# Kernel tuning notes

Hardware: AMD Instinct MI355X
Metric: run time of the kernel (lower is better)

## Reference

```python
import jax, jax.numpy as jnp
import numpy as np

NUM_ITERS = 3
NUM_HEADS = 4
EPS = 1e-8
LN_EPS = 1e-5


def _layernorm(x, w, b):
    mu = jnp.mean(x, axis=-1, keepdims=True)
    var = jnp.mean(jnp.square(x - mu), axis=-1, keepdims=True)
    return (x - mu) * jax.lax.rsqrt(var + LN_EPS) * w + b


def setup_inputs() -> dict:
    key = jax.random.key(0)
    ks = jax.random.split(key, 12)
    B, K, D, Q, Hm = 64, 4096, 256, 8, 512
    s = 0.02
    return {
        "inputs": jax.random.normal(ks[0], (B, K, D), jnp.float32),
        "slots_init": jax.random.normal(ks[1], (B, Q, D), jnp.float32),
        "Wq": jax.random.normal(ks[2], (D, D), jnp.float32) * s,
        "Wk": jax.random.normal(ks[3], (D, D), jnp.float32) * s,
        "Wv": jax.random.normal(ks[4], (D, D), jnp.float32) * s,
        "ln_in_w": jnp.ones((D,), jnp.float32),
        "ln_in_b": jnp.zeros((D,), jnp.float32),
        "ln_slots_w": jnp.ones((D,), jnp.float32),
        "ln_slots_b": jnp.zeros((D,), jnp.float32),
        "ln_mlp_w": jnp.ones((D,), jnp.float32),
        "ln_mlp_b": jnp.zeros((D,), jnp.float32),
        "gru_Wih": jax.random.normal(ks[5], (3 * D, D), jnp.float32) * s,
        "gru_Whh": jax.random.normal(ks[6], (3 * D, D), jnp.float32) * s,
        "gru_bih": jnp.zeros((3 * D,), jnp.float32),
        "gru_bhh": jnp.zeros((3 * D,), jnp.float32),
        "mlp_W1": jax.random.normal(ks[7], (D, Hm), jnp.float32) * s,
        "mlp_b1": jnp.zeros((Hm,), jnp.float32),
        "mlp_W2": jax.random.normal(ks[8], (Hm, D), jnp.float32) * s,
        "mlp_b2": jnp.zeros((D,), jnp.float32),
    }


def reference(inputs, slots_init, Wq, Wk, Wv, ln_in_w, ln_in_b, ln_slots_w,
              ln_slots_b, ln_mlp_w, ln_mlp_b, gru_Wih, gru_Whh, gru_bih,
              gru_bhh, mlp_W1, mlp_b1, mlp_W2, mlp_b2):
    B, K, D = inputs.shape
    Q = slots_init.shape[1]
    H = NUM_HEADS
    dh = D // H
    scale = dh ** -0.5

    x = _layernorm(inputs, ln_in_w, ln_in_b)
    k = (x @ Wk).reshape(B, K, H, dh).transpose(0, 2, 1, 3) * scale  # [B,H,K,dh]
    v = (x @ Wv).reshape(B, K, H, dh).transpose(0, 2, 1, 3)          # [B,H,K,dh]

    slots = slots_init
    attn = None
    for _ in range(NUM_ITERS):
        slots_prev = slots
        s_n = _layernorm(slots, ln_slots_w, ln_slots_b)
        q = (s_n @ Wq).reshape(B, Q, H, dh).transpose(0, 2, 1, 3)    # [B,H,Q,dh]
        logits = jnp.einsum('bhkd,bhqd->bhkq', k, q)                 # [B,H,K,Q]
        # softmax jointly over (heads, slots) per kv position
        attn = jax.nn.softmax(
            logits.transpose(0, 2, 1, 3).reshape(B, K, H * Q), axis=-1
        ).reshape(B, K, H, Q).transpose(0, 2, 1, 3)                  # [B,H,K,Q]
        attn = attn + EPS
        attn = attn / jnp.sum(attn, axis=2, keepdims=True)           # renorm over K
        updates = jnp.einsum('bhkq,bhkd->bqhd', attn, v).reshape(B, Q, D)

        # GRU cell (PyTorch gate order: r, z, n)
        u = updates.reshape(-1, D)
        h = slots_prev.reshape(-1, D)
        gi = u @ gru_Wih.T + gru_bih
        gh = h @ gru_Whh.T + gru_bhh
        i_r, i_z, i_n = jnp.split(gi, 3, axis=-1)
        h_r, h_z, h_n = jnp.split(gh, 3, axis=-1)
        r = jax.nn.sigmoid(i_r + h_r)
        z = jax.nn.sigmoid(i_z + h_z)
        n = jnp.tanh(i_n + r * h_n)
        slots = ((1.0 - z) * n + z * h).reshape(B, Q, D)

        m = _layernorm(slots, ln_mlp_w, ln_mlp_b)
        slots = slots + jax.nn.relu(m @ mlp_W1 + mlp_b1) @ mlp_W2 + mlp_b2

    return slots, attn.mean(axis=1).transpose(0, 2, 1)  # [B,Q,D], [B,Q,K]
```

## Files before the change

kernel.cpp:

```cpp
#include <hip/hip_runtime.h>

#define B   64
#define KK  4096
#define D   256
#define Q   8
#define H   4
#define DH  64
#define HQ  32
#define HM  512
#define NCH 8
#define CHK 512
#define EPS 1e-8f
#define LNE 1e-5f
#define SCALE 0.125f

typedef short bf16x8 __attribute__((ext_vector_type(8)));
typedef float f32x4 __attribute__((ext_vector_type(4)));

__device__ __forceinline__ float bf2f(unsigned short u) {
    unsigned int x = ((unsigned int)u) << 16;
    float f; __builtin_memcpy(&f, &x, 4); return f;
}
__device__ __forceinline__ unsigned short f2bf(float f) {
    unsigned int x; __builtin_memcpy(&x, &f, 4);
    unsigned int lsb = (x >> 16) & 1u;
    x += 0x7fffu + lsb;
    return (unsigned short)(x >> 16);
}

__device__ __forceinline__ void gload16(const void* g, void* l) {
    __builtin_amdgcn_global_load_lds(
        (const __attribute__((address_space(1))) unsigned int*)g,
        (__attribute__((address_space(3))) unsigned int*)l, 16, 0, 0);
}

__device__ __forceinline__ void stage64x512B(const char* src, size_t row0,
                                             size_t stride, char* lds, int w, int l)
{
#pragma unroll
    for (int i = 0; i < 8; ++i) {
        const int seg = w * 8 + i;
        const int r = seg * 2 + (l >> 5);
        const int off = ((l & 31) * 16) ^ ((r & 7) << 4);
        gload16(src + (row0 + r) * stride + off, lds + seg * 1024);
    }
}

__global__ void k_init(const float* __restrict__ s0, float* __restrict__ slots,
                       unsigned short* __restrict__ slots_bf)
{
    const int i = blockIdx.x * 256 + threadIdx.x;
    const float v = s0[i];
    slots[i] = v; slots_bf[i] = f2bf(v);
}

__global__ __launch_bounds__(256) void k0_wkv(
    const float* __restrict__ Wk, const float* __restrict__ Wv,
    unsigned short* __restrict__ WkvT)
{
    const int c = blockIdx.x, d = threadIdx.x;
    const float v = (c < 256) ? Wk[(size_t)d * 256 + c] * SCALE
                              : Wv[(size_t)d * 256 + (c - 256)];
    WkvT[(size_t)c * 256 + d] = f2bf(v);
}

__global__ void k0_cvt(const float* __restrict__ src, unsigned short* __restrict__ dst)
{
    const int i = blockIdx.x * 256 + threadIdx.x;
    dst[i] = f2bf(src[i]);
}

__global__ void k0_t1(const float* __restrict__ W1, unsigned short* __restrict__ W1T)
{
    const int n = blockIdx.x, d = threadIdx.x;
    W1T[(size_t)n * 256 + d] = f2bf(W1[(size_t)d * 512 + n]);
}

__global__ void k0_t2(const float* __restrict__ W2, unsigned short* __restrict__ W2T)
{
    const int n = blockIdx.x, j = threadIdx.x;
    W2T[(size_t)n * 512 + j]       = f2bf(W2[(size_t)j * 256 + n]);
    W2T[(size_t)n * 512 + 256 + j] = f2bf(W2[(size_t)(256 + j) * 256 + n]);
}

__global__ __launch_bounds__(256) void k1_mfma(
    const float* __restrict__ inp, const unsigned short* __restrict__ WkvT,
    const float* __restrict__ lnw, const float* __restrict__ lnb,
    unsigned short* __restrict__ kbuf, unsigned short* __restrict__ vbufT)
{
    __shared__ char smem[65536];
    char* abase = smem;
    char* bb0 = smem + 32768;
    char* bb1 = smem;
    const int t = threadIdx.x, w = t >> 6, l = t & 63;
    const size_t row0 = (size_t)blockIdx.x * 64;

    float4 xv[16];
#pragma unroll
    for (int i = 0; i < 16; ++i)
        xv[i] = ((const float4*)(inp + (row0 + w * 16 + i) * D))[l];
    const float4 w4 = ((const float4*)lnw)[l];
    const float4 b4 = ((const float4*)lnb)[l];
#pragma unroll
    for (int i = 0; i < 16; ++i) {
        const int r = w * 16 + i;
        float4 x = xv[i];
        float s  = x.x + x.y + x.z + x.w;
        float ss = x.x*x.x + x.y*x.y + x.z*x.z + x.w*x.w;
#pragma unroll
        for (int off = 32; off; off >>= 1) { s += __shfl_xor(s, off); ss += __shfl_xor(ss, off); }
        const float mu = s * (1.f / 256.f);
        const float rs = rsqrtf(ss * (1.f / 256.f) - mu * mu + LNE);
        ushort4 pk;
        pk.x = f2bf((x.x - mu) * rs * w4.x + b4.x);
        pk.y = f2bf((x.y - mu) * rs * w4.y + b4.y);
        pk.z = f2bf((x.z - mu) * rs * w4.z + b4.z);
        pk.w = f2bf((x.w - mu) * rs * w4.w + b4.w);
        *(ushort4*)(abase + r * 512 + ((l * 8) ^ ((r & 7) << 4))) = pk;
    }
    __syncthreads();

    const int arow = w * 16 + (l & 15);
    const char* ap = abase + arow * 512;
    const int asw = (l & 7) << 4;
    bf16x8 af[8];
#pragma unroll
    for (int kk = 0; kk < 8; ++kk)
        af[kk] = *(const bf16x8*)(ap + ((kk * 64 + (l >> 4) * 16) ^ asw));

    stage64x512B((const char*)WkvT, 0, 512, bb0, w, l);
    __syncthreads();

    const f32x4 fz = {0.f, 0.f, 0.f, 0.f};
    for (int n2 = 0; n2 < 8; ++n2) {
        if (n2 < 7)
            stage64x512B((const char*)WkvT, (size_t)(n2 + 1) * 64, 512,
                         ((n2 + 1) & 1) ? bb1 : bb0, w, l);
        const char* bbase = (n2 & 1) ? bb1 : bb0;
        f32x4 acc[4] = {fz, fz, fz, fz};
#pragma unroll
        for (int kk = 0; kk < 8; ++kk) {
            const int koff = kk * 64 + (l >> 4) * 16;
#pragma unroll
            for (int nf = 0; nf < 4; ++nf) {
                const int brow = nf * 16 + (l & 15);
                const bf16x8 bf_ = *(const bf16x8*)(bbase + brow * 512 + (koff ^ ((brow & 7) << 4)));
                acc[nf] = __builtin_amdgcn_mfma_f32_16x16x32_bf16(af[kk], bf_, acc[nf], 0, 0, 0);
            }
        }
        const int c0 = n2 * 64;
        const size_t grow0 = row0 + w * 16 + (l >> 4) * 4;
#pragma unroll
        for (int nf = 0; nf < 4; ++nf) {
            const int c = c0 + nf * 16 + (l & 15);
            if (c < 256) {
#pragma unroll
                for (int reg = 0; reg < 4; ++reg)
                    kbuf[(grow0 + reg) * 256 + c] = f2bf(acc[nf][reg]);
            } else {
                const int cc = c - 256;
                const size_t bb = grow0 >> 12;
                const int kl = (int)(grow0 & 4095);
                ushort4 pk;
                pk.x = f2bf(acc[nf][0]); pk.y = f2bf(acc[nf][1]);
                pk.z = f2bf(acc[nf][2]); pk.w = f2bf(acc[nf][3]);
                *(ushort4*)(vbufT + ((bb * 256 + cc) * KK + kl)) = pk;
            }
        }
        __syncthreads();
    }
}

__global__ __launch_bounds__(256) void k2_qproj(
    const float* __restrict__ slots, const float* __restrict__ Wq,
    const float* __restrict__ lnw, const float* __restrict__ lnb, float* __restrict__ qbuf)
{
    const int row = blockIdx.x, t = threadIdx.x;
    __shared__ float sn[256];
    __shared__ float red[8];
    const float x = slots[(size_t)row * D + t];
    float mu, rs;
    {
        float s = x, ss = x * x;
#pragma unroll
        for (int off = 32; off; off >>= 1) { s += __shfl_xor(s, off); ss += __shfl_xor(ss, off); }
        if ((t & 63) == 0) { red[t >> 6] = s; red[4 + (t >> 6)] = ss; }
        __syncthreads();
        const float S  = red[0] + red[1] + red[2] + red[3];
        const float SS = red[4] + red[5] + red[6] + red[7];
        mu = S * (1.f / 256.f);
        rs = rsqrtf(SS * (1.f / 256.f) - mu * mu + LNE);
    }
    sn[t] = (x - mu) * rs * lnw[t] + lnb[t];
    __syncthreads();
    float acc = 0.f;
    for (int d = 0; d < 256; ++d) acc = fmaf(sn[d], Wq[(size_t)d * 256 + t], acc);
    qbuf[(size_t)row * D + t] = acc;
}

__global__ __launch_bounds__(256) void k_attn(
    const unsigned short* __restrict__ kbuf, const unsigned short* __restrict__ vbufT,
    const float* __restrict__ qbuf, float* __restrict__ updp,
    float* __restrict__ denp, float* __restrict__ pbuf, int write_p)
{
    __shared__ unsigned short ksm[64 * 256];
    __shared__ unsigned short vsm[256 * 64];
    __shared__ unsigned short psm[32 * 64];
    __shared__ float dred[4][32];
    const int t = threadIdx.x, w = t >> 6, l = t & 63;
    const int b = blockIdx.x >> 3, chunk = blockIdx.x & 7;
    const int k0g = chunk * CHK;
    const int n = l & 15, lg = l >> 4;

    auto stage_ks = [&](int tile) {
        const size_t rowg = (size_t)b * KK + k0g + tile * 64;
#pragma unroll
        for (int i = 0; i < 8; ++i) {
            const int seg = w * 8 + i;
            const int r = seg * 2 + (l >> 5);
            const int off = ((l & 31) * 16) ^ ((r & 7) << 4);
            gload16((const char*)kbuf + (rowg + r) * 512 + off, (char*)ksm + seg * 1024);
        }
    };
    auto stage_vs = [&](int tile) {
        const int kk0 = k0g + tile * 64;
#pragma unroll
        for (int i = 0; i < 8; ++i) {
            const int seg = w * 8 + i;
            const int d = seg * 8 + (l >> 3);
            const int off = ((l & 7) * 16) ^ ((d & 7) << 4);
            gload16((const char*)vbufT + (((size_t)b * 256 + d) * KK + kk0) * 2 + off,
                    (char*)vsm + seg * 1024);
        }
    };
    stage_ks(0); stage_vs(0);

    bf16x8 qf[2][2];
#pragma unroll
    for (int p = 0; p < 2; ++p) {
        const int h = p * 2 + (n >> 3);
        const float* qb = qbuf + ((size_t)b * Q + (n & 7)) * D;
#pragma unroll
        for (int j = 0; j < 2; ++j) {
            const int dbase = (h * 2 + j) * 32 + lg * 8;
            short tmp[8];
#pragma unroll
            for (int e = 0; e < 8; ++e) tmp[e] = (short)f2bf(qb[dbase + e]);
            __builtin_memcpy(&qf[p][j], tmp, 16);
        }
    }
    const bf16x8 ZV = {0,0,0,0,0,0,0,0};
    const f32x4 fz = {0.f,0.f,0.f,0.f};
    f32x4 pv[2][4];
#pragma unroll
    for (int mt = 0; mt < 2; ++mt)
#pragma unroll
        for (int nf = 0; nf < 4; ++nf) pv[mt][nf] = fz;
    float den0 = 0.f, den1 = 0.f;

    for (int tile = 0; tile < 8; ++tile) {
        __syncthreads();
        const int arow = w * 16 + n;
        const char* ap = (const char*)ksm + arow * 512;
        const int asw = (arow & 7) << 4;
        f32x4 lac[2] = {fz, fz};
#pragma unroll
        for (int kk = 0; kk < 8; ++kk) {
            const bf16x8 a = *(const bf16x8*)(ap + ((kk * 64 + lg * 16) ^ asw));
            const int p = kk >> 2;
            const bool on = (((kk & 3) >> 1) == (n >> 3));
            const bf16x8 bq = on ? qf[p][kk & 1] : ZV;
            if (p == 0) lac[0] = __builtin_amdgcn_mfma_f32_16x16x32_bf16(a, bq, lac[0], 0, 0, 0);
            else        lac[1] = __builtin_amdgcn_mfma_f32_16x16x32_bf16(a, bq, lac[1], 0, 0, 0);
        }
#pragma unroll
        for (int reg = 0; reg < 4; ++reg) {
            float m = fmaxf(lac[0][reg], lac[1][reg]);
#pragma unroll
            for (int off = 8; off; off >>= 1) m = fmaxf(m, __shfl_xor(m, off));
            const float e0 = __expf(lac[0][reg] - m);
            const float e1 = __expf(lac[1][reg] - m);
            float se = e0 + e1;
#pragma unroll
            for (int off = 8; off; off >>= 1) se += __shfl_xor(se, off);
            const float inv = 1.f / se;
            lac[0][reg] = e0 * inv; lac[1][reg] = e1 * inv;
            den0 += lac[0][reg];    den1 += lac[1][reg];
        }
        const int kb = w * 16 + lg * 4;
        {
            ushort4 p0, p1;
            p0.x = f2bf(lac[0][0]); p0.y = f2bf(lac[0][1]); p0.z = f2bf(lac[0][2]); p0.w = f2bf(lac[0][3]);
            p1.x = f2bf(lac[1][0]); p1.y = f2bf(lac[1][1]); p1.z = f2bf(lac[1][2]); p1.w = f2bf(lac[1][3]);
            *(ushort4*)((char*)psm + n * 128 + ((kb * 2) ^ ((n & 7) << 4))) = p0;
            *(ushort4*)((char*)psm + (16 + n) * 128 + ((kb * 2) ^ ((n & 7) << 4))) = p1;
        }
        if (write_p) {
            float* pp = pbuf + ((size_t)b * KK + k0g + tile * 64 + kb) * HQ;
#pragma unroll
            for (int reg = 0; reg < 4; ++reg) {
                pp[(size_t)reg * HQ + n] = lac[0][reg];
                pp[(size_t)reg * HQ + 16 + n] = lac[1][reg];
            }
        }
        __syncthreads();
        if (tile < 7) stage_ks(tile + 1);
#pragma unroll
        for (int kk = 0; kk < 2; ++kk) {
            const int koff = kk * 64 + lg * 16;
            const bf16x8 a0 = *(const bf16x8*)((char*)psm + n * 128 + (koff ^ ((n & 7) << 4)));
            const bf16x8 a1 = *(const bf16x8*)((char*)psm + (16 + n) * 128 + (koff ^ ((n & 7) << 4)));
#pragma unroll
            for (int nf = 0; nf < 4; ++nf) {
                const int d = w * 64 + nf * 16 + n;
                const bf16x8 bv = *(const bf16x8*)((char*)vsm + d * 128 + (koff ^ ((d & 7) << 4)));
                pv[0][nf] = __builtin_amdgcn_mfma_f32_16x16x32_bf16(a0, bv, pv[0][nf], 0, 0, 0);
                pv[1][nf] = __builtin_amdgcn_mfma_f32_16x16x32_bf16(a1, bv, pv[1][nf], 0, 0, 0);
            }
        }
        __syncthreads();
        if (tile < 7) stage_vs(tile + 1);
    }

    den0 += __shfl_xor(den0, 16); den0 += __shfl_xor(den0, 32);
    den1 += __shfl_xor(den1, 16); den1 += __shfl_xor(den1, 32);
    if (l < 16) { dred[w][l] = den0; dred[w][16 + l] = den1; }
    __syncthreads();
    if (t < 32)
        denp[((size_t)b * NCH + chunk) * HQ + t] =
            dred[0][t] + dred[1][t] + dred[2][t] + dred[3][t];

    if ((lg >> 1) == (w & 1)) {
        const int mt = w >> 1;
#pragma unroll
        for (int nf = 0; nf < 4; ++nf) {
#pragma unroll
            for (int reg = 0; reg < 4; ++reg) {
                const int q = (lg & 1) * 4 + reg;
                updp[(((size_t)b * NCH + chunk) * Q + q) * D + w * 64 + nf * 16 + n] = pv[mt][nf][reg];
            }
        }
    }
}

__global__ __launch_bounds__(256) void k_reduce(
    const float* __restrict__ updp, const float* __restrict__ denp,
    unsigned short* __restrict__ updbf)
{
    const int row = blockIdx.x, t = threadIdx.x;
    const int b = row >> 3, q = row & 7, h = t >> 6;
    float ds = 0.f, us = 0.f;
#pragma unroll
    for (int c = 0; c < NCH; ++c) {
        ds += denp[((size_t)b * NCH + c) * HQ + h * Q + q];
        us += updp[(((size_t)b * NCH + c) * Q + q) * D + t];
    }
    updbf[(size_t)row * D + t] = f2bf(us / (ds + (float)KK * EPS));
}

__global__ void k_den(const float* __restrict__ denp, float* __restrict__ invden)
{
    const int b = blockIdx.x, t = threadIdx.x;
    float s = 0.f;
#pragma unroll
    for (int c = 0; c < NCH; ++c) s += denp[((size_t)b * NCH + c) * HQ + t];
    invden[b * HQ + t] = 1.f / (s + (float)KK * EPS);
}

__global__ __launch_bounds__(256) void k_gru(
    const unsigned short* __restrict__ updbf, const unsigned short* __restrict__ slotsbf,
    const unsigned short* __restrict__ Wihbf, const unsigned short* __restrict__ Whhbf,
    float* __restrict__ gg)
{
    __shared__ unsigned short As[64 * 256];
    __shared__ unsigned short Bs[64 * 256];
    const int t = threadIdx.x, w = t >> 6, l = t & 63;
    const int rb = blockIdx.x / 24, nb = blockIdx.x % 24;
    const unsigned short* Asrc = (nb < 12) ? updbf : slotsbf;
    stage64x512B((const char*)Asrc, (size_t)rb * 64, 512, (char*)As, w, l);
    if (nb < 12) stage64x512B((const char*)Wihbf, (size_t)nb * 64, 512, (char*)Bs, w, l);
    else         stage64x512B((const char*)Whhbf, (size_t)(nb - 12) * 64, 512, (char*)Bs, w, l);
    __syncthreads();
    const int arow = w * 16 + (l & 15);
    const int asw = (l & 7) << 4;
    bf16x8 af[8];
#pragma unroll
    for (int kk = 0; kk < 8; ++kk)
        af[kk] = *(const bf16x8*)((char*)As + arow * 512 + ((kk * 64 + (l >> 4) * 16) ^ asw));
    const f32x4 fz = {0.f,0.f,0.f,0.f};
    f32x4 acc[4] = {fz, fz, fz, fz};
#pragma unroll
    for (int kk = 0; kk < 8; ++kk) {
        const int koff = kk * 64 + (l >> 4) * 16;
#pragma unroll
        for (int nf = 0; nf < 4; ++nf) {
            const int brow = nf * 16 + (l & 15);
            const bf16x8 bf_ = *(const bf16x8*)((char*)Bs + brow * 512 + (koff ^ ((brow & 7) << 4)));
            acc[nf] = __builtin_amdgcn_mfma_f32_16x16x32_bf16(af[kk], bf_, acc[nf], 0, 0, 0);
        }
    }
    const int colbase = (nb < 12) ? nb * 64 : 768 + (nb - 12) * 64;
#pragma unroll
    for (int nf = 0; nf < 4; ++nf) {
        const int col = colbase + nf * 16 + (l & 15);
#pragma unroll
        for (int reg = 0; reg < 4; ++reg) {
            const size_t row = (size_t)rb * 64 + w * 16 + (l >> 4) * 4 + reg;
            gg[row * 1536 + col] = acc[nf][reg];
        }
    }
}

__global__ __launch_bounds__(256) void k_gates(
    const float* __restrict__ gg, const float* __restrict__ slots,
    const float* __restrict__ bih, const float* __restrict__ bhh,
    const float* __restrict__ lnw, const float* __restrict__ lnb,
    float* __restrict__ snew, unsigned short* __restrict__ mbf)
{
    const int row = blockIdx.x, t = threadIdx.x;
    __shared__ float red[8];
    const float* g = gg + (size_t)row * 1536;
    const float i_r = g[t]        + bih[t];
    const float i_z = g[256 + t]  + bih[256 + t];
    const float i_n = g[512 + t]  + bih[512 + t];
    const float h_r = g[768 + t]  + bhh[t];
    const float h_z = g[1024 + t] + bhh[256 + t];
    const float h_n = g[1280 + t] + bhh[512 + t];
    const float r = 1.f / (1.f + __expf(-(i_r + h_r)));
    const float z = 1.f / (1.f + __expf(-(i_z + h_z)));
    const float nn = tanhf(i_n + r * h_n);
    const float h0 = slots[(size_t)row * D + t];
    const float sn = (1.f - z) * nn + z * h0;
    snew[(size_t)row * D + t] = sn;
    float mu, rs;
    {
        float s = sn, ss = sn * sn;
#pragma unroll
        for (int off = 32; off; off >>= 1) { s += __shfl_xor(s, off); ss += __shfl_xor(ss, off); }
        if ((t & 63) == 0) { red[t >> 6] = s; red[4 + (t >> 6)] = ss; }
        __syncthreads();
        const float S  = red[0] + red[1] + red[2] + red[3];
        const float SS = red[4] + red[5] + red[6] + red[7];
        mu = S * (1.f / 256.f);
        rs = rsqrtf(SS * (1.f / 256.f) - mu * mu + LNE);
    }
    mbf[(size_t)row * D + t] = f2bf((sn - mu) * rs * lnw[t] + lnb[t]);
}

__global__ __launch_bounds__(256) void k_mlp1(
    const unsigned short* __restrict__ mbf, const unsigned short* __restrict__ W1T,
    const float* __restrict__ b1, unsigned short* __restrict__ hidbf)
{
    __shared__ unsigned short As[64 * 256];
    __shared__ unsigned short Bs[64 * 256];
    const int t = threadIdx.x, w = t >> 6, l = t & 63;
    const int rb = blockIdx.x >> 3, nb = blockIdx.x & 7;
    stage64x512B((const char*)mbf, (size_t)rb * 64, 512, (char*)As, w, l);
    stage64x512B((const char*)W1T, (size_t)nb * 64, 512, (char*)Bs, w, l);
    __syncthreads();
    const int arow = w * 16 + (l & 15);
    const int asw = (l & 7) << 4;
    bf16x8 af[8];
#pragma unroll
    for (int kk = 0; kk < 8; ++kk)
        af[kk] = *(const bf16x8*)((char*)As + arow * 512 + ((kk * 64 + (l >> 4) * 16) ^ asw));
    const f32x4 fz = {0.f,0.f,0.f,0.f};
    f32x4 acc[4] = {fz, fz, fz, fz};
#pragma unroll
    for (int kk = 0; kk < 8; ++kk) {
        const int koff = kk * 64 + (l >> 4) * 16;
#pragma unroll
        for (int nf = 0; nf < 4; ++nf) {
            const int brow = nf * 16 + (l & 15);
            const bf16x8 bf_ = *(const bf16x8*)((char*)Bs + brow * 512 + (koff ^ ((brow & 7) << 4)));
            acc[nf] = __builtin_amdgcn_mfma_f32_16x16x32_bf16(af[kk], bf_, acc[nf], 0, 0, 0);
        }
    }
#pragma unroll
    for (int nf = 0; nf < 4; ++nf) {
        const int col = nb * 64 + nf * 16 + (l & 15);
        const float bb = b1[col];
#pragma unroll
        for (int reg = 0; reg < 4; ++reg) {
            const size_t row = (size_t)rb * 64 + w * 16 + (l >> 4) * 4 + reg;
            hidbf[row * HM + col] = f2bf(fmaxf(acc[nf][reg] + bb, 0.f));
        }
    }
}

__global__ __launch_bounds__(256) void k_mlp2(
    const unsigned short* __restrict__ hidbf, const unsigned short* __restrict__ W2T,
    const float* __restrict__ b2, const float* __restrict__ snew,
    float* __restrict__ slots, unsigned short* __restrict__ slotsbf)
{
    __shared__ unsigned short As[64 * 256];
    __shared__ unsigned short Bs[64 * 256];
    const int t = threadIdx.x, w = t >> 6, l = t & 63;
    const int rb = blockIdx.x >> 2, nb = blockIdx.x & 3;
    const f32x4 fz = {0.f,0.f,0.f,0.f};
    f32x4 acc[4] = {fz, fz, fz, fz};
    for (int c = 0; c < 2; ++c) {
        stage64x512B((const char*)hidbf + c * 512, (size_t)rb * 64, 1024, (char*)As, w, l);
        stage64x512B((const char*)W2T + c * 512, (size_t)nb * 64, 1024, (char*)Bs, w, l);
        __syncthreads();
        const int arow = w * 16 + (l & 15);
        const int asw = (l & 7) << 4;
        bf16x8 af[8];
#pragma unroll
        for (int kk = 0; kk < 8; ++kk)
            af[kk] = *(const bf16x8*)((char*)As + arow * 512 + ((kk * 64 + (l >> 4) * 16) ^ asw));
#pragma unroll
        for (int kk = 0; kk < 8; ++kk) {
            const int koff = kk * 64 + (l >> 4) * 16;
#pragma unroll
            for (int nf = 0; nf < 4; ++nf) {
                const int brow = nf * 16 + (l & 15);
                const bf16x8 bf_ = *(const bf16x8*)((char*)Bs + brow * 512 + (koff ^ ((brow & 7) << 4)));
                acc[nf] = __builtin_amdgcn_mfma_f32_16x16x32_bf16(af[kk], bf_, acc[nf], 0, 0, 0);
            }
        }
        __syncthreads();
    }
#pragma unroll
    for (int nf = 0; nf < 4; ++nf) {
        const int col = nb * 64 + nf * 16 + (l & 15);
        const float bb = b2[col];
#pragma unroll
        for (int reg = 0; reg < 4; ++reg) {
            const size_t row = (size_t)rb * 64 + w * 16 + (l >> 4) * 4 + reg;
            const float v = snew[row * D + col] + acc[nf][reg] + bb;
            slots[row * D + col] = v;
            slotsbf[row * D + col] = f2bf(v);
        }
    }
}

__global__ void k7_copy(const float* __restrict__ s, float* __restrict__ o)
{
    const int i = blockIdx.x * 256 + threadIdx.x;
    o[i] = s[i];
}

__global__ __launch_bounds__(256) void k7_attnout(
    const float* __restrict__ pbuf, const float* __restrict__ invden, float* __restrict__ out2)
{
    const int blk = blockIdx.x;
    const int b = blk >> 4;
    const int kk0 = (blk & 15) * 256;
    __shared__ float ps[256][33];
    __shared__ float inv[32];
    const int t = threadIdx.x;
    const float* pp = pbuf + ((size_t)b * KK + kk0) * HQ;
    for (int i = 0; i < 32; ++i) {
        const int idx = i * 256 + t;
        ps[idx >> 5][idx & 31] = pp[idx];
    }
    if (t < 32) inv[t] = invden[b * HQ + t];
// ... 22 lines not shown
    const float* ln_in_b = (const float*)d_in[6];
    const float* ln_s_w  = (const float*)d_in[7];
    const float* ln_s_b  = (const float*)d_in[8];
    const float* ln_m_w  = (const float*)d_in[9];
    const float* ln_m_b  = (const float*)d_in[10];
    const float* gWih    = (const float*)d_in[11];
    const float* gWhh    = (const float*)d_in[12];
    const float* gbih    = (const float*)d_in[13];
    const float* gbhh    = (const float*)d_in[14];
    const float* W1      = (const float*)d_in[15];
    const float* b1      = (const float*)d_in[16];
    const float* W2      = (const float*)d_in[17];
    const float* b2      = (const float*)d_in[18];

    char* p = (char*)d_ws;
    unsigned short* kbuf  = (unsigned short*)p; p += (size_t)B * KK * D * 2;
    unsigned short* vbufT = (unsigned short*)p; p += (size_t)B * KK * D * 2;
    float* pbuf   = (float*)p; p += (size_t)B * KK * HQ * 4;
    float* updp   = (float*)p; p += (size_t)B * NCH * Q * D * 4;
    float* denp   = (float*)p; p += (size_t)B * NCH * HQ * 4;
    float* invden = (float*)p; p += (size_t)B * HQ * 4;
    float* qbuf   = (float*)p; p += (size_t)B * Q * D * 4;
    float* slots  = (float*)p; p += (size_t)B * Q * D * 4;
    float* snew   = (float*)p; p += (size_t)B * Q * D * 4;
    unsigned short* slots_bf = (unsigned short*)p; p += (size_t)B * Q * D * 2;
    unsigned short* upd_bf   = (unsigned short*)p; p += (size_t)B * Q * D * 2;
    unsigned short* mbf      = (unsigned short*)p; p += (size_t)B * Q * D * 2;
    unsigned short* hidbf    = (unsigned short*)p; p += (size_t)B * Q * HM * 2;
    unsigned short* WkvT     = (unsigned short*)p; p += (size_t)512 * 256 * 2;
    unsigned short* Wihbf    = (unsigned short*)p; p += (size_t)768 * 256 * 2;
    unsigned short* Whhbf    = (unsigned short*)p; p += (size_t)768 * 256 * 2;
    unsigned short* W1T      = (unsigned short*)p; p += (size_t)HM * 256 * 2;
    unsigned short* W2T      = (unsigned short*)p; p += (size_t)256 * HM * 2;
    float* gg = updp;

    k_init<<<(B * Q * D) / 256, 256, 0, stream>>>(slots0, slots, slots_bf);
    k0_wkv<<<512, 256, 0, stream>>>(Wk, Wv, WkvT);
    k0_cvt<<<768, 256, 0, stream>>>(gWih, Wihbf);
    k0_cvt<<<768, 256, 0, stream>>>(gWhh, Whhbf);
    k0_t1<<<512, 256, 0, stream>>>(W1, W1T);
    k0_t2<<<256, 256, 0, stream>>>(W2, W2T);
    k1_mfma<<<(B * KK) / 64, 256, 0, stream>>>(inputs, WkvT, ln_in_w, ln_in_b, kbuf, vbufT);
    for (int it = 0; it < 3; ++it) {
        k2_qproj<<<B * Q, 256, 0, stream>>>(slots, Wq, ln_s_w, ln_s_b, qbuf);
        k_attn<<<B * NCH, 256, 0, stream>>>(kbuf, vbufT, qbuf, updp, denp, pbuf, (it == 2) ? 1 : 0);
        k_reduce<<<B * Q, 256, 0, stream>>>(updp, denp, upd_bf);
        k_gru<<<8 * 24, 256, 0, stream>>>(upd_bf, slots_bf, Wihbf, Whhbf, gg);
        k_gates<<<B * Q, 256, 0, stream>>>(gg, slots, gbih, gbhh, ln_m_w, ln_m_b, snew, mbf);
        k_mlp1<<<8 * 8, 256, 0, stream>>>(mbf, W1T, b1, hidbf);
        k_mlp2<<<8 * 4, 256, 0, stream>>>(hidbf, W2T, b2, snew, slots, slots_bf);
    }
    k_den<<<B, 32, 0, stream>>>(denp, invden);
    k7_copy<<<(B * Q * D) / 256, 256, 0, stream>>>(slots, (float*)d_out);
    k7_attnout<<<B * (KK / 256), 256, 0, stream>>>(pbuf, invden, (float*)d_out + (size_t)B * Q * D);
}
```

Measured before the change: 464.2 us.

## Fuse slot-update chain into one kernel and restructure attention loads

Folds the per-iteration reduce, GRU GEMMs, gates, MLP, and next-iteration Q projection into a single k_slot kernel of 32 blocks, replacing six launches per iteration. The attention kernel now uses 16 chunks of 256 keys and reads K and V fragments straight from global memory instead of staging them through LDS. The K/V projection kernel uses 32-column B tiles with a deeper prefetch and less shared memory. The aim is to cut launch overhead and intermediate global round-trips and raise attention parallelism, at the cost of a low-parallelism fused slot kernel and uncoalesced direct global loads in attention.

```diff
diff --git a/kernel.cpp b/kernel.cpp
--- a/kernel.cpp
+++ b/kernel.cpp
@@ -8,14 +8,16 @@
 #define DH  64
 #define HQ  32
 #define HM  512
-#define NCH 8
-#define CHK 512
+#define NCH 16
+#define CHK 256
 #define EPS 1e-8f
 #define LNE 1e-5f
 #define SCALE 0.125f
 
 typedef short bf16x8 __attribute__((ext_vector_type(8)));
 typedef float f32x4 __attribute__((ext_vector_type(4)));
+
+#define MFMA __builtin_amdgcn_mfma_f32_16x16x32_bf16
 
 __device__ __forceinline__ float bf2f(unsigned short u) {
     unsigned int x = ((unsigned int)u) << 16;
@@ -34,24 +36,10 @@
         (__attribute__((address_space(3))) unsigned int*)l, 16, 0, 0);
 }
 
-__device__ __forceinline__ void stage64x512B(const char* src, size_t row0,
-                                             size_t stride, char* lds, int w, int l)
-{
-#pragma unroll
-    for (int i = 0; i < 8; ++i) {
-        const int seg = w * 8 + i;
-        const int r = seg * 2 + (l >> 5);
-        const int off = ((l & 31) * 16) ^ ((r & 7) << 4);
-        gload16(src + (row0 + r) * stride + off, lds + seg * 1024);
-    }
-}
-
-__global__ void k_init(const float* __restrict__ s0, float* __restrict__ slots,
-                       unsigned short* __restrict__ slots_bf)
+__global__ void k_init(const float* __restrict__ s0, float* __restrict__ slots)
 {
     const int i = blockIdx.x * 256 + threadIdx.x;
-    const float v = s0[i];
-    slots[i] = v; slots_bf[i] = f2bf(v);
+    slots[i] = s0[i];
 }
 
 __global__ __launch_bounds__(256) void k0_wkv(
@@ -72,15 +60,21 @@
 
 __global__ void k0_t1(const float* __restrict__ W1, unsigned short* __restrict__ W1T)
 {
-    const int n = blockIdx.x, d = threadIdx.x;
-    W1T[(size_t)n * 256 + d] = f2bf(W1[(size_t)d * 512 + n]);
+    const int nn = blockIdx.x, d = threadIdx.x;
+    W1T[(size_t)nn * 256 + d] = f2bf(W1[(size_t)d * 512 + nn]);
 }
 
 __global__ void k0_t2(const float* __restrict__ W2, unsigned short* __restrict__ W2T)
 {
-    const int n = blockIdx.x, j = threadIdx.x;
-    W2T[(size_t)n * 512 + j]       = f2bf(W2[(size_t)j * 256 + n]);
-    W2T[(size_t)n * 512 + 256 + j] = f2bf(W2[(size_t)(256 + j) * 256 + n]);
+    const int nn = blockIdx.x, j = threadIdx.x;
+    W2T[(size_t)nn * 512 + j]       = f2bf(W2[(size_t)j * 256 + nn]);
+    W2T[(size_t)nn * 512 + 256 + j] = f2bf(W2[(size_t)(256 + j) * 256 + nn]);
+}
+
+__global__ void k0_wq(const float* __restrict__ Wq, unsigned short* __restrict__ WqT)
+{
+    const int nn = blockIdx.x, d = threadIdx.x;
+    WqT[(size_t)nn * 256 + d] = f2bf(Wq[(size_t)d * 256 + nn]);
 }
 
 __global__ __launch_bounds__(256) void k1_mfma(
@@ -88,12 +82,23 @@
     const float* __restrict__ lnw, const float* __restrict__ lnb,
     unsigned short* __restrict__ kbuf, unsigned short* __restrict__ vbufT)
 {
-    __shared__ char smem[65536];
+    __shared__ char smem[49152];
     char* abase = smem;
     char* bb0 = smem + 32768;
     char* bb1 = smem;
     const int t = threadIdx.x, w = t >> 6, l = t & 63;
     const size_t row0 = (size_t)blockIdx.x * 64;
+
+    auto stageB = [&](int n2, char* dst) {
+#pragma unroll
+        for (int i = 0; i < 4; ++i) {
+            const int seg = w * 4 + i;
+            const int r = seg * 2 + (l >> 5);
+            const int off = ((l & 31) * 16) ^ ((r & 7) << 4);
+            gload16((const char*)WkvT + ((size_t)n2 * 32 + r) * 512 + off, dst + seg * 1024);
+        }
+    };
+    stageB(0, bb0);
 
     float4 xv[16];
 #pragma unroll
@@ -127,31 +132,27 @@
 #pragma unroll
     for (int kk = 0; kk < 8; ++kk)
         af[kk] = *(const bf16x8*)(ap + ((kk * 64 + (l >> 4) * 16) ^ asw));
-
-    stage64x512B((const char*)WkvT, 0, 512, bb0, w, l);
-    __syncthreads();
+    __syncthreads();
+    stageB(1, bb1);
 
     const f32x4 fz = {0.f, 0.f, 0.f, 0.f};
-    for (int n2 = 0; n2 < 8; ++n2) {
-        if (n2 < 7)
-            stage64x512B((const char*)WkvT, (size_t)(n2 + 1) * 64, 512,
-                         ((n2 + 1) & 1) ? bb1 : bb0, w, l);
+    for (int n2 = 0; n2 < 16; ++n2) {
         const char* bbase = (n2 & 1) ? bb1 : bb0;
-        f32x4 acc[4] = {fz, fz, fz, fz};
+        f32x4 acc[2] = {fz, fz};
 #pragma unroll
         for (int kk = 0; kk < 8; ++kk) {
             const int koff = kk * 64 + (l >> 4) * 16;
 #pragma unroll
-            for (int nf = 0; nf < 4; ++nf) {
+            for (int nf = 0; nf < 2; ++nf) {
                 const int brow = nf * 16 + (l & 15);
                 const bf16x8 bf_ = *(const bf16x8*)(bbase + brow * 512 + (koff ^ ((brow & 7) << 4)));
-                acc[nf] = __builtin_amdgcn_mfma_f32_16x16x32_bf16(af[kk], bf_, acc[nf], 0, 0, 0);
-            }
-        }
-        const int c0 = n2 * 64;
+                acc[nf] = MFMA(af[kk], bf_, acc[nf], 0, 0, 0);
+            }
+        }
+        const int c0 = n2 * 32;
         const size_t grow0 = row0 + w * 16 + (l >> 4) * 4;
 #pragma unroll
-        for (int nf = 0; nf < 4; ++nf) {
+        for (int nf = 0; nf < 2; ++nf) {
             const int c = c0 + nf * 16 + (l & 15);
             if (c < 256) {
 #pragma unroll
@@ -168,6 +169,7 @@
             }
         }
         __syncthreads();
+        if (n2 < 14) stageB(n2 + 2, (n2 & 1) ? bb1 : bb0);
     }
 }
 
@@ -203,37 +205,12 @@
     const float* __restrict__ qbuf, float* __restrict__ updp,
     float* __restrict__ denp, float* __restrict__ pbuf, int write_p)
 {
-    __shared__ unsigned short ksm[64 * 256];
-    __shared__ unsigned short vsm[256 * 64];
     __shared__ unsigned short psm[32 * 64];
     __shared__ float dred[4][32];
     const int t = threadIdx.x, w = t >> 6, l = t & 63;
-    const int b = blockIdx.x >> 3, chunk = blockIdx.x & 7;
+    const int b = blockIdx.x >> 4, chunk = blockIdx.x & 15;
     const int k0g = chunk * CHK;
     const int n = l & 15, lg = l >> 4;
-
-    auto stage_ks = [&](int tile) {
-        const size_t rowg = (size_t)b * KK + k0g + tile * 64;
-#pragma unroll
-        for (int i = 0; i < 8; ++i) {
-            const int seg = w * 8 + i;
-            const int r = seg * 2 + (l >> 5);
-            const int off = ((l & 31) * 16) ^ ((r & 7) << 4);
-            gload16((const char*)kbuf + (rowg + r) * 512 + off, (char*)ksm + seg * 1024);
-        }
-    };
-    auto stage_vs = [&](int tile) {
-        const int kk0 = k0g + tile * 64;
-#pragma unroll
-        for (int i = 0; i < 8; ++i) {
-            const int seg = w * 8 + i;
-            const int d = seg * 8 + (l >> 3);
-            const int off = ((l & 7) * 16) ^ ((d & 7) << 4);
-            gload16((const char*)vbufT + (((size_t)b * 256 + d) * KK + kk0) * 2 + off,
-                    (char*)vsm + seg * 1024);
-        }
-    };
-    stage_ks(0); stage_vs(0);
 
     bf16x8 qf[2][2];
 #pragma unroll
@@ -258,20 +235,21 @@
         for (int nf = 0; nf < 4; ++nf) pv[mt][nf] = fz;
     float den0 = 0.f, den1 = 0.f;
 
-    for (int tile = 0; tile < 8; ++tile) {
-        __syncthreads();
-        const int arow = w * 16 + n;
-        const char* ap = (const char*)ksm + arow * 512;
-        const int asw = (arow & 7) << 4;
+    const unsigned short* kbase = kbuf + ((size_t)b * KK + k0g + w * 16 + n) * 256 + lg * 8;
+
+    for (int tile = 0; tile < 4; ++tile) {
+        bf16x8 kf[8];
+#pragma unroll
+        for (int kk = 0; kk < 8; ++kk)
+            kf[kk] = *(const bf16x8*)(kbase + (size_t)tile * 64 * 256 + kk * 32);
         f32x4 lac[2] = {fz, fz};
 #pragma unroll
         for (int kk = 0; kk < 8; ++kk) {
-            const bf16x8 a = *(const bf16x8*)(ap + ((kk * 64 + lg * 16) ^ asw));
             const int p = kk >> 2;
             const bool on = (((kk & 3) >> 1) == (n >> 3));
             const bf16x8 bq = on ? qf[p][kk & 1] : ZV;
-            if (p == 0) lac[0] = __builtin_amdgcn_mfma_f32_16x16x32_bf16(a, bq, lac[0], 0, 0, 0);
-            else        lac[1] = __builtin_amdgcn_mfma_f32_16x16x32_bf16(a, bq, lac[1], 0, 0, 0);
+            if (p == 0) lac[0] = MFMA(kf[kk], bq, lac[0], 0, 0, 0);
+            else        lac[1] = MFMA(kf[kk], bq, lac[1], 0, 0, 0);
         }
 #pragma unroll
         for (int reg = 0; reg < 4; ++reg) {
@@ -287,6 +265,7 @@
             lac[0][reg] = e0 * inv; lac[1][reg] = e1 * inv;
             den0 += lac[0][reg];    den1 += lac[1][reg];
         }
+        __syncthreads();
         const int kb = w * 16 + lg * 4;
         {
             ushort4 p0, p1;
@@ -304,22 +283,20 @@
             }
         }
         __syncthreads();
-        if (tile < 7) stage_ks(tile + 1);
-#pragma unroll
-        for (int kk = 0; kk < 2; ++kk) {
-            const int koff = kk * 64 + lg * 16;
+#pragma unroll
+        for (int kkp = 0; kkp < 2; ++kkp) {
+            const int koff = kkp * 64 + lg * 16;
             const bf16x8 a0 = *(const bf16x8*)((char*)psm + n * 128 + (koff ^ ((n & 7) << 4)));
             const bf16x8 a1 = *(const bf16x8*)((char*)psm + (16 + n) * 128 + (koff ^ ((n & 7) << 4)));
 #pragma unroll
             for (int nf = 0; nf < 4; ++nf) {
                 const int d = w * 64 + nf * 16 + n;
-                const bf16x8 bv = *(const bf16x8*)((char*)vsm + d * 128 + (koff ^ ((d & 7) << 4)));
-                pv[0][nf] = __builtin_amdgcn_mfma_f32_16x16x32_bf16(a0, bv, pv[0][nf], 0, 0, 0);
-                pv[1][nf] = __builtin_amdgcn_mfma_f32_16x16x32_bf16(a1, bv, pv[1][nf], 0, 0, 0);
-            }
-        }
-        __syncthreads();
-        if (tile < 7) stage_vs(tile + 1);
+                const bf16x8 bv = *(const bf16x8*)(vbufT + ((size_t)b * 256 + d) * KK
+                                                   + k0g + tile * 64 + kkp * 32 + lg * 8);
+                pv[0][nf] = MFMA(a0, bv, pv[0][nf], 0, 0, 0);
+                pv[1][nf] = MFMA(a1, bv, pv[1][nf], 0, 0, 0);
+            }
+        }
     }
 
     den0 += __shfl_xor(den0, 16); den0 += __shfl_xor(den0, 32);
@@ -343,19 +320,253 @@
     }
 }
 
-__global__ __launch_bounds__(256) void k_reduce(
+__device__ __forceinline__ void ln_rows(const f32x4 sv[4], char* dstA, float* red,
+    const float* __restrict__ lnw, const float* __restrict__ lnb,
+    int w, int n, int lg, int col0)
+{
+    float ps[4], pq[4];
+#pragma unroll
+    for (int r = 0; r < 4; ++r) {
+        float s = 0.f, q2 = 0.f;
+#pragma unroll
+        for (int nf = 0; nf < 4; ++nf) { const float v = sv[nf][r]; s += v; q2 += v * v; }
+#pragma unroll
+        for (int off = 1; off < 16; off <<= 1) { s += __shfl_xor(s, off); q2 += __shfl_xor(q2, off); }
+        ps[r] = s; pq[r] = q2;
+    }
+    if (n == 0) {
+#pragma unroll
+        for (int r = 0; r < 4; ++r) {
+            red[(lg * 4 + r) * 8 + w * 2]     = ps[r];
+            red[(lg * 4 + r) * 8 + w * 2 + 1] = pq[r];
+        }
+    }
+    __syncthreads();
+    float mu[4], rs[4];
+#pragma unroll
+    for (int r = 0; r < 4; ++r) {
+        const int rowm = lg * 4 + r;
+        const float S  = red[rowm*8+0] + red[rowm*8+2] + red[rowm*8+4] + red[rowm*8+6];
+        const float SS = red[rowm*8+1] + red[rowm*8+3] + red[rowm*8+5] + red[rowm*8+7];
+        mu[r] = S * (1.f / 256.f);
+        rs[r] = rsqrtf(SS * (1.f / 256.f) - mu[r] * mu[r] + LNE);
+    }
+#pragma unroll
+    for (int nf = 0; nf < 4; ++nf) {
+        const int col = col0 + nf * 16;
+        const float wv = lnw[col], bv = lnb[col];
+#pragma unroll
+        for (int r = 0; r < 4; ++r) {
+            const int rowm = lg * 4 + r;
+            const float mval = (sv[nf][r] - mu[r]) * rs[r] * wv + bv;
+            *(unsigned short*)(dstA + rowm * 512 + ((col * 2) ^ ((rowm & 7) << 4))) = f2bf(mval);
+        }
+    }
+}
+
+__global__ __launch_bounds__(256) void k_slot(
     const float* __restrict__ updp, const float* __restrict__ denp,
-    unsigned short* __restrict__ updbf)
-{
-    const int row = blockIdx.x, t = threadIdx.x;
-    const int b = row >> 3, q = row & 7, h = t >> 6;
-    float ds = 0.f, us = 0.f;
-#pragma unroll
-    for (int c = 0; c < NCH; ++c) {
-        ds += denp[((size_t)b * NCH + c) * HQ + h * Q + q];
-        us += updp[(((size_t)b * NCH + c) * Q + q) * D + t];
-    }
-    updbf[(size_t)row * D + t] = f2bf(us / (ds + (float)KK * EPS));
+    float* __restrict__ slots,
+    const unsigned short* __restrict__ Wihbf, const unsigned short* __restrict__ Whhbf,
+    const float* __restrict__ bih, const float* __restrict__ bhh,
+    const unsigned short* __restrict__ W1T, const float* __restrict__ b1,
+    const unsigned short* __restrict__ W2T, const float* __restrict__ b2,
+    const float* __restrict__ lnmw, const float* __restrict__ lnmb,
+    const unsigned short* __restrict__ WqT,
+    const float* __restrict__ lnsw, const float* __restrict__ lnsb,
+    float* __restrict__ qbuf)
+{
+    __shared__ char sm[34304];
+    unsigned short* uA = (unsigned short*)(sm);
+    unsigned short* hA = (unsigned short*)(sm + 8192);
+    float* hf32        = (float*)(sm + 16384);
+    char*  hidA        = sm + 16384;
+    float* dsum        = (float*)(sm + 33280);
+    float* red         = (float*)(sm + 33536);
+    const int t = threadIdx.x, w = t >> 6, l = t & 63;
+    const int n = l & 15, lg = l >> 4;
+    const int R0 = blockIdx.x * 16;
+    const f32x4 fz = {0.f, 0.f, 0.f, 0.f};
+
+    {
+        float us[16];
+#pragma unroll
+        for (int m = 0; m < 16; ++m) {
+            const int gr = R0 + m, bb = gr >> 3, q = gr & 7;
+            float s = 0.f;
+#pragma unroll
+            for (int c = 0; c < 16; ++c)
+                s += updp[(((size_t)(bb * 16 + c)) * 8 + q) * 256 + t];
+            us[m] = s;
+        }
+        if (t < 64) {
+            const int m = t >> 2, h = t & 3;
+            const int gr = R0 + m, bb = gr >> 3, q = gr & 7;
+            float s = 0.f;
+#pragma unroll
+            for (int c = 0; c < 16; ++c)
+                s += denp[(size_t)(bb * 16 + c) * 32 + h * 8 + q];
+            dsum[m * 4 + h] = s;
+        }
+#pragma unroll
+        for (int m = 0; m < 16; ++m) {
+            const float hv = slots[(size_t)(R0 + m) * 256 + t];
+            hf32[m * 264 + t] = hv;
+            *(unsigned short*)((char*)hA + m * 512 + ((t * 2) ^ ((m & 7) << 4))) = f2bf(hv);
+        }
+        __syncthreads();
+        const int h = t >> 6;
+#pragma unroll
+        for (int m = 0; m < 16; ++m) {
+            const float inv = 1.f / (dsum[m * 4 + h] + (float)KK * EPS);
+            *(unsigned short*)((char*)uA + m * 512 + ((t * 2) ^ ((m & 7) << 4))) = f2bf(us[m] * inv);
+        }
+    }
+    __syncthreads();
+
+    f32x4 sv[4];
+    {
+        f32x4 ai0[4], ai1[4], ai2[4];
+#pragma unroll
+        for (int nf = 0; nf < 4; ++nf) { ai0[nf] = fz; ai1[nf] = fz; ai2[nf] = fz; }
+#pragma unroll
+        for (int kk = 0; kk < 8; ++kk) {
+            const bf16x8 au = *(const bf16x8*)((char*)uA + n * 512 + ((kk * 64 + lg * 16) ^ ((n & 7) << 4)));
+            const int kidx = kk * 32 + lg * 8;
+#pragma unroll
+            for (int nf = 0; nf < 4; ++nf) {
+                const int col = w * 64 + nf * 16 + n;
+                const bf16x8 br = *(const bf16x8*)(Wihbf + (size_t)col * 256 + kidx);
+                const bf16x8 bz = *(const bf16x8*)(Wihbf + (size_t)(256 + col) * 256 + kidx);
+                const bf16x8 bn = *(const bf16x8*)(Wihbf + (size_t)(512 + col) * 256 + kidx);
+                ai0[nf] = MFMA(au, br, ai0[nf], 0, 0, 0);
+                ai1[nf] = MFMA(au, bz, ai1[nf], 0, 0, 0);
+                ai2[nf] = MFMA(au, bn, ai2[nf], 0, 0, 0);
+            }
+        }
+        f32x4 ah0[4], ah1[4], ah2[4];
+#pragma unroll
+        for (int nf = 0; nf < 4; ++nf) { ah0[nf] = fz; ah1[nf] = fz; ah2[nf] = fz; }
+#pragma unroll
+        for (int kk = 0; kk < 8; ++kk) {
+            const bf16x8 ah_ = *(const bf16x8*)((char*)hA + n * 512 + ((kk * 64 + lg * 16) ^ ((n & 7) << 4)));
+            const int kidx = kk * 32 + lg * 8;
+#pragma unroll
+            for (int nf = 0; nf < 4; ++nf) {
+                const int col = w * 64 + nf * 16 + n;
+                const bf16x8 cr = *(const bf16x8*)(Whhbf + (size_t)col * 256 + kidx);
+                const bf16x8 cz = *(const bf16x8*)(Whhbf + (size_t)(256 + col) * 256 + kidx);
+                const bf16x8 cn = *(const bf16x8*)(Whhbf + (size_t)(512 + col) * 256 + kidx);
+                ah0[nf] = MFMA(ah_, cr, ah0[nf], 0, 0, 0);
+                ah1[nf] = MFMA(ah_, cz, ah1[nf], 0, 0, 0);
+                ah2[nf] = MFMA(ah_, cn, ah2[nf], 0, 0, 0);
+            }
+        }
+#pragma unroll
+        for (int nf = 0; nf < 4; ++nf) {
+            const int col = w * 64 + nf * 16 + n;
+            const float br_ = bih[col], bz_ = bih[256 + col], bn_ = bih[512 + col];
+            const float cr_ = bhh[col], cz_ = bhh[256 + col], cn_ = bhh[512 + col];
+#pragma unroll
+            for (int r = 0; r < 4; ++r) {
+                const int rowm = lg * 4 + r;
+                const float ir = ai0[nf][r] + br_, iz = ai1[nf][r] + bz_, inn = ai2[nf][r] + bn_;
+                const float hr = ah0[nf][r] + cr_, hz = ah1[nf][r] + cz_, hn = ah2[nf][r] + cn_;
+                const float rg = 1.f / (1.f + __expf(-(ir + hr)));
+                const float zg = 1.f / (1.f + __expf(-(iz + hz)));
+                const float ng = tanhf(inn + rg * hn);
+                const float h0v = hf32[rowm * 264 + col];
+                sv[nf][r] = (1.f - zg) * ng + zg * h0v;
+            }
+        }
+    }
+    ln_rows(sv, (char*)uA, red, lnmw, lnmb, w, n, lg, w * 64 + n);
+    __syncthreads();
+
+    {
+        f32x4 m1[8];
+#pragma unroll
+        for (int nf = 0; nf < 8; ++nf) m1[nf] = fz;
+#pragma unroll
+        for (int kk = 0; kk < 8; ++kk) {
+            const bf16x8 a = *(const bf16x8*)((char*)uA + n * 512 + ((kk * 64 + lg * 16) ^ ((n & 7) << 4)));
+            const int kidx = kk * 32 + lg * 8;
+#pragma unroll
+            for (int nf = 0; nf < 8; ++nf) {
+                const int colh = w * 128 + nf * 16 + n;
+                const bf16x8 bb = *(const bf16x8*)(W1T + (size_t)colh * 256 + kidx);
+                m1[nf] = MFMA(a, bb, m1[nf], 0, 0, 0);
+            }
+        }
+        __syncthreads();
+#pragma unroll
+        for (int nf = 0; nf < 8; ++nf) {
+            const int colh = w * 128 + nf * 16 + n;
+            const float bb = b1[colh];
+#pragma unroll
+            for (int r = 0; r < 4; ++r) {
+                const int rowm = lg * 4 + r;
+                *(unsigned short*)(hidA + rowm * 1024 + ((colh * 2) ^ ((rowm & 7) << 4)))
+                    = f2bf(fmaxf(m1[nf][r] + bb, 0.f));
+            }
+        }
+    }
+    __syncthreads();
+
+    {
+        f32x4 m2[4];
+#pragma unroll
+        for (int nf = 0; nf < 4; ++nf) m2[nf] = fz;
+#pragma unroll
+        for (int kk = 0; kk < 16; ++kk) {
+            const bf16x8 a = *(const bf16x8*)(hidA + n * 1024 + ((kk * 64 + lg * 16) ^ ((n & 7) << 4)));
+            const int kidx = kk * 32 + lg * 8;
+#pragma unroll
+            for (int nf = 0; nf < 4; ++nf) {
+                const int col = w * 64 + nf * 16 + n;
+                const bf16x8 bb = *(const bf16x8*)(W2T + (size_t)col * 512 + kidx);
+                m2[nf] = MFMA(a, bb, m2[nf], 0, 0, 0);
+            }
+        }
+#pragma unroll
+        for (int nf = 0; nf < 4; ++nf) {
+            const int col = w * 64 + nf * 16 + n;
+            const float bb = b2[col];
+#pragma unroll
+            for (int r = 0; r < 4; ++r) {
+                const int rowm = lg * 4 + r;
+                const float v = m2[nf][r] + bb + sv[nf][r];
+                sv[nf][r] = v;
+                slots[(size_t)(R0 + rowm) * 256 + col] = v;
+            }
+        }
+    }
+    ln_rows(sv, (char*)hA, red, lnsw, lnsb, w, n, lg, w * 64 + n);
+    __syncthreads();
+
+    {
+        f32x4 qa[4];
+#pragma unroll
+        for (int nf = 0; nf < 4; ++nf) qa[nf] = fz;
+#pragma unroll
+        for (int kk = 0; kk < 8; ++kk) {
+            const bf16x8 a = *(const bf16x8*)((char*)hA + n * 512 + ((kk * 64 + lg * 16) ^ ((n & 7) << 4)));
+            const int kidx = kk * 32 + lg * 8;
+#pragma unroll
+            for (int nf = 0; nf < 4; ++nf) {
+                const int col = w * 64 + nf * 16 + n;
+                const bf16x8 bb = *(const bf16x8*)(WqT + (size_t)col * 256 + kidx);
+                qa[nf] = MFMA(a, bb, qa[nf], 0, 0, 0);
+            }
+        }
+#pragma unroll
+        for (int nf = 0; nf < 4; ++nf) {
+            const int col = w * 64 + nf * 16 + n;
+#pragma unroll
+            for (int r = 0; r < 4; ++r)
+                qbuf[(size_t)(R0 + lg * 4 + r) * 256 + col] = qa[nf][r];
+        }
+    }
 }
 
 __global__ void k_den(const float* __restrict__ denp, float* __restrict__ invden)
@@ -365,174 +576,6 @@
 #pragma unroll
     for (int c = 0; c < NCH; ++c) s += denp[((size_t)b * NCH + c) * HQ + t];
     invden[b * HQ + t] = 1.f / (s + (float)KK * EPS);
-}
-
-__global__ __launch_bounds__(256) void k_gru(
-    const unsigned short* __restrict__ updbf, const unsigned short* __restrict__ slotsbf,
-    const unsigned short* __restrict__ Wihbf, const unsigned short* __restrict__ Whhbf,
-    float* __restrict__ gg)
-{
-    __shared__ unsigned short As[64 * 256];
-    __shared__ unsigned short Bs[64 * 256];
-    const int t = threadIdx.x, w = t >> 6, l = t & 63;
-    const int rb = blockIdx.x / 24, nb = blockIdx.x % 24;
-    const unsigned short* Asrc = (nb < 12) ? updbf : slotsbf;
-    stage64x512B((const char*)Asrc, (size_t)rb * 64, 512, (char*)As, w, l);
-    if (nb < 12) stage64x512B((const char*)Wihbf, (size_t)nb * 64, 512, (char*)Bs, w, l);
-    else         stage64x512B((const char*)Whhbf, (size_t)(nb - 12) * 64, 512, (char*)Bs, w, l);
-    __syncthreads();
-    const int arow = w * 16 + (l & 15);
-    const int asw = (l & 7) << 4;
-    bf16x8 af[8];
-#pragma unroll
-    for (int kk = 0; kk < 8; ++kk)
-        af[kk] = *(const bf16x8*)((char*)As + arow * 512 + ((kk * 64 + (l >> 4) * 16) ^ asw));
-    const f32x4 fz = {0.f,0.f,0.f,0.f};
-    f32x4 acc[4] = {fz, fz, fz, fz};
-#pragma unroll
-    for (int kk = 0; kk < 8; ++kk) {
-        const int koff = kk * 64 + (l >> 4) * 16;
-#pragma unroll
-        for (int nf = 0; nf < 4; ++nf) {
-            const int brow = nf * 16 + (l & 15);
-            const bf16x8 bf_ = *(const bf16x8*)((char*)Bs + brow * 512 + (koff ^ ((brow & 7) << 4)));
-            acc[nf] = __builtin_amdgcn_mfma_f32_16x16x32_bf16(af[kk], bf_, acc[nf], 0, 0, 0);
-        }
-    }
-    const int colbase = (nb < 12) ? nb * 64 : 768 + (nb - 12) * 64;
-#pragma unroll
-    for (int nf = 0; nf < 4; ++nf) {
-        const int col = colbase + nf * 16 + (l & 15);
-#pragma unroll
-        for (int reg = 0; reg < 4; ++reg) {
-            const size_t row = (size_t)rb * 64 + w * 16 + (l >> 4) * 4 + reg;
-            gg[row * 1536 + col] = acc[nf][reg];
-        }
-    }
-}
-
-__global__ __launch_bounds__(256) void k_gates(
-    const float* __restrict__ gg, const float* __restrict__ slots,
-    const float* __restrict__ bih, const float* __restrict__ bhh,
-    const float* __restrict__ lnw, const float* __restrict__ lnb,
-    float* __restrict__ snew, unsigned short* __restrict__ mbf)
-{
-    const int row = blockIdx.x, t = threadIdx.x;
-    __shared__ float red[8];
-    const float* g = gg + (size_t)row * 1536;
-    const float i_r = g[t]        + bih[t];
-    const float i_z = g[256 + t]  + bih[256 + t];
-    const float i_n = g[512 + t]  + bih[512 + t];
-    const float h_r = g[768 + t]  + bhh[t];
-    const float h_z = g[1024 + t] + bhh[256 + t];
-    const float h_n = g[1280 + t] + bhh[512 + t];
-    const float r = 1.f / (1.f + __expf(-(i_r + h_r)));
-    const float z = 1.f / (1.f + __expf(-(i_z + h_z)));
-    const float nn = tanhf(i_n + r * h_n);
-    const float h0 = slots[(size_t)row * D + t];
-    const float sn = (1.f - z) * nn + z * h0;
-    snew[(size_t)row * D + t] = sn;
-    float mu, rs;
-    {
-        float s = sn, ss = sn * sn;
-#pragma unroll
-        for (int off = 32; off; off >>= 1) { s += __shfl_xor(s, off); ss += __shfl_xor(ss, off); }
-        if ((t & 63) == 0) { red[t >> 6] = s; red[4 + (t >> 6)] = ss; }
-        __syncthreads();
-        const float S  = red[0] + red[1] + red[2] + red[3];
-        const float SS = red[4] + red[5] + red[6] + red[7];
-        mu = S * (1.f / 256.f);
-        rs = rsqrtf(SS * (1.f / 256.f) - mu * mu + LNE);
-    }
-    mbf[(size_t)row * D + t] = f2bf((sn - mu) * rs * lnw[t] + lnb[t]);
-}
-
-__global__ __launch_bounds__(256) void k_mlp1(
-    const unsigned short* __restrict__ mbf, const unsigned short* __restrict__ W1T,
-    const float* __restrict__ b1, unsigned short* __restrict__ hidbf)
-{
-    __shared__ unsigned short As[64 * 256];
-    __shared__ unsigned short Bs[64 * 256];
-    const int t = threadIdx.x, w = t >> 6, l = t & 63;
-    const int rb = blockIdx.x >> 3, nb = blockIdx.x & 7;
-    stage64x512B((const char*)mbf, (size_t)rb * 64, 512, (char*)As, w, l);
-    stage64x512B((const char*)W1T, (size_t)nb * 64, 512, (char*)Bs, w, l);
-    __syncthreads();
-    const int arow = w * 16 + (l & 15);
-    const int asw = (l & 7) << 4;
-    bf16x8 af[8];
-#pragma unroll
-    for (int kk = 0; kk < 8; ++kk)
-        af[kk] = *(const bf16x8*)((char*)As + arow * 512 + ((kk * 64 + (l >> 4) * 16) ^ asw));
-    const f32x4 fz = {0.f,0.f,0.f,0.f};
-    f32x4 acc[4] = {fz, fz, fz, fz};
-#pragma unroll
-    for (int kk = 0; kk < 8; ++kk) {
-        const int koff = kk * 64 + (l >> 4) * 16;
-#pragma unroll
-        for (int nf = 0; nf < 4; ++nf) {
-            const int brow = nf * 16 + (l & 15);
-            const bf16x8 bf_ = *(const bf16x8*)((char*)Bs + brow * 512 + (koff ^ ((brow & 7) << 4)));
-            acc[nf] = __builtin_amdgcn_mfma_f32_16x16x32_bf16(af[kk], bf_, acc[nf], 0, 0, 0);
-        }
-    }
-#pragma unroll
-    for (int nf = 0; nf < 4; ++nf) {
-        const int col = nb * 64 + nf * 16 + (l & 15);
-        const float bb = b1[col];
-#pragma unroll
-        for (int reg = 0; reg < 4; ++reg) {
-            const size_t row = (size_t)rb * 64 + w * 16 + (l >> 4) * 4 + reg;
-            hidbf[row * HM + col] = f2bf(fmaxf(acc[nf][reg] + bb, 0.f));
-        }
-    }
-}
-
-__global__ __launch_bounds__(256) void k_mlp2(
-    const unsigned short* __restrict__ hidbf, const unsigned short* __restrict__ W2T,
-    const float* __restrict__ b2, const float* __restrict__ snew,
-    float* __restrict__ slots, unsigned short* __restrict__ slotsbf)
-{
-    __shared__ unsigned short As[64 * 256];
-    __shared__ unsigned short Bs[64 * 256];
-    const int t = threadIdx.x, w = t >> 6, l = t & 63;
-    const int rb = blockIdx.x >> 2, nb = blockIdx.x & 3;
-    const f32x4 fz = {0.f,0.f,0.f,0.f};
-    f32x4 acc[4] = {fz, fz, fz, fz};
-    for (int c = 0; c < 2; ++c) {
-        stage64x512B((const char*)hidbf + c * 512, (size_t)rb * 64, 1024, (char*)As, w, l);
-        stage64x512B((const char*)W2T + c * 512, (size_t)nb * 64, 1024, (char*)Bs, w, l);
-        __syncthreads();
-        const int arow = w * 16 + (l & 15);
-        const int asw = (l & 7) << 4;
-        bf16x8 af[8];
-#pragma unroll
-        for (int kk = 0; kk < 8; ++kk)
-            af[kk] = *(const bf16x8*)((char*)As + arow * 512 + ((kk * 64 + (l >> 4) * 16) ^ asw));
-#pragma unroll
-        for (int kk = 0; kk < 8; ++kk) {
-            const int koff = kk * 64 + (l >> 4) * 16;
-#pragma unroll
-            for (int nf = 0; nf < 4; ++nf) {
-                const int brow = nf * 16 + (l & 15);
-                const bf16x8 bf_ = *(const bf16x8*)((char*)Bs + brow * 512 + (koff ^ ((brow & 7) << 4)));
-                acc[nf] = __builtin_amdgcn_mfma_f32_16x16x32_bf16(af[kk], bf_, acc[nf], 0, 0, 0);
-            }
-        }
-        __syncthreads();
-    }
-#pragma unroll
-    for (int nf = 0; nf < 4; ++nf) {
-        const int col = nb * 64 + nf * 16 + (l & 15);
-        const float bb = b2[col];
-#pragma unroll
-        for (int reg = 0; reg < 4; ++reg) {
-            const size_t row = (size_t)rb * 64 + w * 16 + (l >> 4) * 4 + reg;
-            const float v = snew[row * D + col] + acc[nf][reg] + bb;
-            slots[row * D + col] = v;
-            slotsbf[row * D + col] = f2bf(v);
-        }
-    }
 }
 
 __global__ void k7_copy(const float* __restrict__ s, float* __restrict__ o)
@@ -601,33 +644,27 @@
     float* invden = (float*)p; p += (size_t)B * HQ * 4;
     float* qbuf   = (float*)p; p += (size_t)B * Q * D * 4;
     float* slots  = (float*)p; p += (size_t)B * Q * D * 4;
-    float* snew   = (float*)p; p += (size_t)B * Q * D * 4;
-    unsigned short* slots_bf = (unsigned short*)p; p += (size_t)B * Q * D * 2;
-    unsigned short* upd_bf   = (unsigned short*)p; p += (size_t)B * Q * D * 2;
-    unsigned short* mbf      = (unsigned short*)p; p += (size_t)B * Q * D * 2;
-    unsigned short* hidbf    = (unsigned short*)p; p += (size_t)B * Q * HM * 2;
-    unsigned short* WkvT     = (unsigned short*)p; p += (size_t)512 * 256 * 2;
-    unsigned short* Wihbf    = (unsigned short*)p; p += (size_t)768 * 256 * 2;
-    unsigned short* Whhbf    = (unsigned short*)p; p += (size_t)768 * 256 * 2;
-    unsigned short* W1T      = (unsigned short*)p; p += (size_t)HM * 256 * 2;
-    unsigned short* W2T      = (unsigned short*)p; p += (size_t)256 * HM * 2;
-    float* gg = updp;
-
-    k_init<<<(B * Q * D) / 256, 256, 0, stream>>>(slots0, slots, slots_bf);
+    unsigned short* WkvT  = (unsigned short*)p; p += (size_t)512 * 256 * 2;
+    unsigned short* Wihbf = (unsigned short*)p; p += (size_t)768 * 256 * 2;
+    unsigned short* Whhbf = (unsigned short*)p; p += (size_t)768 * 256 * 2;
+    unsigned short* W1T   = (unsigned short*)p; p += (size_t)HM * 256 * 2;
+    unsigned short* W2T   = (unsigned short*)p; p += (size_t)256 * HM * 2;
+    unsigned short* WqT   = (unsigned short*)p; p += (size_t)256 * 256 * 2;
+
+    k_init<<<(B * Q * D) / 256, 256, 0, stream>>>(slots0, slots);
     k0_wkv<<<512, 256, 0, stream>>>(Wk, Wv, WkvT);
     k0_cvt<<<768, 256, 0, stream>>>(gWih, Wihbf);
     k0_cvt<<<768, 256, 0, stream>>>(gWhh, Whhbf);
     k0_t1<<<512, 256, 0, stream>>>(W1, W1T);
     k0_t2<<<256, 256, 0, stream>>>(W2, W2T);
+    k0_wq<<<256, 256, 0, stream>>>(Wq, WqT);
     k1_mfma<<<(B * KK) / 64, 256, 0, stream>>>(inputs, WkvT, ln_in_w, ln_in_b, kbuf, vbufT);
+    k2_qproj<<<B * Q, 256, 0, stream>>>(slots, Wq, ln_s_w, ln_s_b, qbuf);
     for (int it = 0; it < 3; ++it) {
-        k2_qproj<<<B * Q, 256, 0, stream>>>(slots, Wq, ln_s_w, ln_s_b, qbuf);
         k_attn<<<B * NCH, 256, 0, stream>>>(kbuf, vbufT, qbuf, updp, denp, pbuf, (it == 2) ? 1 : 0);
-        k_reduce<<<B * Q, 256, 0, stream>>>(updp, denp, upd_bf);
-        k_gru<<<8 * 24, 256, 0, stream>>>(upd_bf, slots_bf, Wihbf, Whhbf, gg);
-        k_gates<<<B * Q, 256, 0, stream>>>(gg, slots, gbih, gbhh, ln_m_w, ln_m_b, snew, mbf);
-        k_mlp1<<<8 * 8, 256, 0, stream>>>(mbf, W1T, b1, hidbf);
-        k_mlp2<<<8 * 4, 256, 0, stream>>>(hidbf, W2T, b2, snew, slots, slots_bf);
+        k_slot<<<32, 256, 0, stream>>>(updp, denp, slots, Wihbf, Whhbf, gbih, gbhh,
+                                       W1T, b1, W2T, b2, ln_m_w, ln_m_b, WqT,
+                                       ln_s_w, ln_s_b, qbuf);
     }
     k_den<<<B, 32, 0, stream>>>(denp, invden);
     k7_copy<<<(B * Q * D) / 256, 256, 0, stream>>>(slots, (float*)d_out);
```

Result: slower. 585.4 us (+26.1%).
